# Kernel tuning notes

Measured on AMD Instinct MI355X. Metric: run time of the kernel, lower is better.

Reference implementation:

```python
import jax, jax.numpy as jnp
import numpy as np

N = 100_000   # nodes
E = 1_600_000 # edges (avg degree 16)
IN_DIM = 128
OUT_DIM = 64
NEG_SLOPE = 0.2  # PyG GATConv default


def setup_inputs() -> dict:
    key = jax.random.key(0)
    k_x, k_ei, k_w, k_as, k_ad = jax.random.split(key, 5)
    x = jax.random.normal(k_x, (N, IN_DIM), dtype=jnp.float32)
    edge_index = jax.random.randint(k_ei, (2, E), 0, N, dtype=jnp.int32)
    # GATConv params (heads=1): linear weight, attention vectors, output bias
    W = jax.random.normal(k_w, (IN_DIM, OUT_DIM), dtype=jnp.float32) / np.sqrt(IN_DIM)
    a_src = jax.random.normal(k_as, (OUT_DIM,), dtype=jnp.float32) * 0.1
    a_dst = jax.random.normal(k_ad, (OUT_DIM,), dtype=jnp.float32) * 0.1
    bias = jnp.zeros((OUT_DIM,), dtype=jnp.float32)
    return {"x": x, "edge_index": edge_index, "W": W, "a_src": a_src, "a_dst": a_dst, "bias": bias}


def reference(x, edge_index, W, a_src, a_dst, bias):
    # PyG GATConv, heads=1, add_self_loops=True
    h = x @ W                                   # [N, OUT]
    loop = jnp.arange(N, dtype=edge_index.dtype)
    ei = jnp.concatenate([edge_index, jnp.stack([loop, loop])], axis=1)  # [2, E+N]
    src, dst = ei[0], ei[1]
    # per-node attention logits, gathered per edge
    alpha_s = h @ a_src                         # [N]
    alpha_d = h @ a_dst                         # [N]
    e = alpha_s[src] + alpha_d[dst]             # [E+N]
    e = jnp.where(e > 0, e, NEG_SLOPE * e)      # leaky_relu
    # segment softmax over edges sharing the same destination node
    m = jax.ops.segment_max(e, dst, num_segments=N)   # every node has a self loop
    ex = jnp.exp(e - m[dst])
    s = jax.ops.segment_sum(ex, dst, num_segments=N)
    alpha = ex / s[dst]                         # [E+N]
    # weighted scatter-add of source messages
    out = jax.ops.segment_sum(alpha[:, None] * h[src], dst, num_segments=N)  # [N, OUT]
    return out + bias
```

## Files before the change

### kernel.cpp

```cpp
#include <hip/hip_runtime.h>
#include <hip/hip_bf16.h>

#ifndef NEG_SLOPE
#define NEG_SLOPE 0.2f
#endif

#define GRP_SHIFT 9
#define GRP_SIZE 512
#define NGMAX 256
#define MS_CHUNK 4096
#define BKT_CAP 10240

typedef short bf16x8 __attribute__((ext_vector_type(8)));
typedef float f32x4 __attribute__((ext_vector_type(4)));

__device__ __forceinline__ unsigned short f2bf(float f) {
    union { float f; unsigned int u; } c; c.f = f;
    unsigned int r = (c.u + 0x7FFFu + ((c.u >> 16) & 1u)) >> 16;
    return (unsigned short)r;
}
__device__ __forceinline__ float bf2f(unsigned short u) {
    union { unsigned int u; float f; } c; c.u = ((unsigned int)u) << 16;
    return c.f;
}
__device__ __forceinline__ float bflo(unsigned int u) {
    union { unsigned int u; float f; } c; c.u = u << 16;
    return c.f;
}
__device__ __forceinline__ float bfhi(unsigned int u) {
    union { unsigned int u; float f; } c; c.u = u & 0xffff0000u;
    return c.f;
}

struct GemmSmem {
    unsigned short xb[64 * 136];
    unsigned short wt[64 * 136];
};
struct MsSmem {
    unsigned int pack[MS_CHUNK];
    unsigned char gtag[MS_CHUNK];
    int hist[NGMAX];
    int gb[NGMAX];
    int wsum[4];
};
union FusedSmem {
    GemmSmem g;
    MsSmem m;
};

__global__ __launch_bounds__(256) void gemm_ms_kernel(
    const float* __restrict__ x, const float* __restrict__ W,
    const float* __restrict__ a_src, const float* __restrict__ a_dst,
    unsigned short* __restrict__ hb, float* __restrict__ as_,
    float* __restrict__ ad_, const int* __restrict__ ei,
    int* __restrict__ cursor, unsigned int* __restrict__ pairs,
    int N, int E, int NG, int nchunk)
{
    __shared__ FusedSmem sm;
    const int tid = threadIdx.x;

    if ((int)blockIdx.x < nchunk) {
        unsigned int* ls_pack = sm.m.pack;
        unsigned char* ls_g = sm.m.gtag;
        int* ls_hist = sm.m.hist;
        int* ls_gb = sm.m.gb;
        int* ls_wsum = sm.m.wsum;

        const int cs = (int)blockIdx.x * MS_CHUNK;
        const int n = min(MS_CHUNK, E - cs);
        const int* srcp = ei + cs;
        const int* dstp = ei + E + cs;

        ls_hist[tid] = 0;
        __syncthreads();
        for (int i = tid; i < n; i += 256)
            atomicAdd(&ls_hist[dstp[i] >> GRP_SHIFT], 1);
        __syncthreads();

        const int h = ls_hist[tid];
        const int lane = tid & 63;
        int incl = h;
#pragma unroll
        for (int off = 1; off < 64; off <<= 1) {
            const int t = __shfl_up(incl, off);
            if (lane >= off) incl += t;
        }
        const int wv = tid >> 6;
        if (lane == 63) ls_wsum[wv] = incl;
        __syncthreads();
        int wpre = 0;
        for (int w = 0; w < wv; ++w) wpre += ls_wsum[w];
        const int excl = wpre + incl - h;
        if (tid < NG && h > 0) {
            const int old = atomicAdd(&cursor[tid], h);
            ls_gb[tid] = tid * BKT_CAP + old - excl;
        }
        __syncthreads();
        ls_hist[tid] = excl;
        __syncthreads();

        for (int i = tid; i < n; i += 256) {
            const int src = srcp[i];
            const int dst = dstp[i];
            const int g = dst >> GRP_SHIFT;
            const int idx = atomicAdd(&ls_hist[g], 1);
            ls_pack[idx] = ((unsigned int)src << GRP_SHIFT) | (unsigned int)(dst & (GRP_SIZE - 1));
            ls_g[idx] = (unsigned char)g;
        }
        __syncthreads();

        for (int i = tid; i < n; i += 256) {
            const int g = ls_g[i];
            const int pos = ls_gb[g] + i;
            if (pos < (g + 1) * BKT_CAP)
                pairs[pos] = ls_pack[i];
        }
    } else {
        unsigned short* xb = sm.g.xb;
        unsigned short* wt = sm.g.wt;
        const int r0 = ((int)blockIdx.x - nchunk) * 64;

        for (int idx = tid; idx < 2048; idx += 256) {
            const int r = idx >> 5;
            const int c4 = idx & 31;
            const int row = r0 + r;
            float4 v = make_float4(0.f, 0.f, 0.f, 0.f);
            if (row < N) v = ((const float4*)(x + (size_t)row * 128))[c4];
            ushort4 o;
            o.x = f2bf(v.x); o.y = f2bf(v.y); o.z = f2bf(v.z); o.w = f2bf(v.w);
            *(ushort4*)(xb + r * 136 + c4 * 4) = o;
        }
        {
            const int n = tid & 63;
            const int kb = (tid >> 6) * 32;
            for (int kk = 0; kk < 32; ++kk) {
                const int k = kb + kk;
                wt[n * 136 + k] = f2bf(W[k * 64 + n]);
            }
        }
        __syncthreads();

        const int wv = tid >> 6;
        const int lane = tid & 63;
        const int m16 = lane & 15;
        const int quad = lane >> 4;

        f32x4 acc[4];
#pragma unroll
        for (int ct = 0; ct < 4; ++ct) acc[ct] = (f32x4){0.f, 0.f, 0.f, 0.f};

        const unsigned short* xrow = xb + (wv * 16 + m16) * 136;
#pragma unroll
        for (int kq = 0; kq < 4; ++kq) {
            const int k0 = kq * 32;
            const bf16x8 a = *(const bf16x8*)(xrow + k0 + quad * 8);
#pragma unroll
            for (int ct = 0; ct < 4; ++ct) {
                const bf16x8 b = *(const bf16x8*)(wt + (ct * 16 + m16) * 136 + k0 + quad * 8);
                acc[ct] = __builtin_amdgcn_mfma_f32_16x16x32_bf16(a, b, acc[ct], 0, 0, 0);
            }
        }

#pragma unroll
        for (int ct = 0; ct < 4; ++ct) {
#pragma unroll
            for (int rg = 0; rg < 4; ++rg) {
                const int row = r0 + wv * 16 + quad * 4 + rg;
                if (row < N) hb[(size_t)row * 64 + ct * 16 + m16] = f2bf(acc[ct][rg]);
            }
        }

        float asv[4], adv[4];
#pragma unroll
        for (int ct = 0; ct < 4; ++ct) {
            asv[ct] = a_src[ct * 16 + m16];
            adv[ct] = a_dst[ct * 16 + m16];
        }
#pragma unroll
        for (int rg = 0; rg < 4; ++rg) {
            float ps = acc[0][rg] * asv[0] + acc[1][rg] * asv[1] +
                       acc[2][rg] * asv[2] + acc[3][rg] * asv[3];
            float pd = acc[0][rg] * adv[0] + acc[1][rg] * adv[1] +
                       acc[2][rg] * adv[2] + acc[3][rg] * adv[3];
#pragma unroll
            for (int off = 1; off < 16; off <<= 1) {
                ps += __shfl_xor(ps, off);
                pd += __shfl_xor(pd, off);
            }
            const int row = r0 + wv * 16 + quad * 4 + rg;
            if (m16 == 0 && row < N) { as_[row] = ps; ad_[row] = pd; }
        }
    }
}

__global__ __launch_bounds__(1024) void group_sort_kernel(
    const unsigned int* __restrict__ pairs, const int* __restrict__ cursor,
    unsigned int* __restrict__ meta, int* __restrict__ csr, int N)
{
    __shared__ int sdeg[GRP_SIZE];
    __shared__ int scur[GRP_SIZE];
    __shared__ int swsum[8];
    __shared__ int ssrc[BKT_CAP];
    const int g = blockIdx.x;
    const int tid = threadIdx.x;
    const int eb0 = g * BKT_CAP;
    const int cnt = min(cursor[g], BKT_CAP);

    if (tid < GRP_SIZE) sdeg[tid] = 0;
    __syncthreads();
    for (int i = tid; i < cnt; i += 1024)
        atomicAdd(&sdeg[pairs[eb0 + i] & (GRP_SIZE - 1)], 1);
    __syncthreads();

    int s = 0, incl = 0;
    if (tid < GRP_SIZE) {
        s = sdeg[tid];
        const int lane = tid & 63;
        incl = s;
#pragma unroll
        for (int off = 1; off < 64; off <<= 1) {
            const int t = __shfl_up(incl, off);
            if (lane >= off) incl += t;
        }
        if (lane == 63) swsum[tid >> 6] = incl;
    }
    __syncthreads();
    if (tid < GRP_SIZE) {
        int wpre = 0;
        const int wv = tid >> 6;
        for (int w = 0; w < wv; ++w) wpre += swsum[w];
        const int excl = wpre + incl - s;
        scur[tid] = excl;
        const int node = (g << GRP_SHIFT) + tid;
        if (node < N)
            meta[node] = ((unsigned int)(eb0 + excl) << 10) | (unsigned int)min(s, 1023);
    }
    __syncthreads();

    for (int i = tid; i < cnt; i += 1024) {
        const unsigned int p = pairs[eb0 + i];
        const int idx = atomicAdd(&scur[p & (GRP_SIZE - 1)], 1);
        ssrc[idx] = (int)(p >> GRP_SHIFT);
    }
    __syncthreads();
    for (int i = tid; i < cnt; i += 1024)
        csr[eb0 + i] = ssrc[i];
}

__device__ void aggregate_slow(
    const unsigned short* __restrict__ h, const float* __restrict__ as_,
    const float* __restrict__ ad_, const int* __restrict__ csr,
    const float* __restrict__ bias, float* __restrict__ out,
    int wid, int p0, int deg, int lane)
{
    const float adi = ad_[wid];
    float e0 = as_[wid] + adi;
    e0 = e0 > 0.f ? e0 : NEG_SLOPE * e0;
    float m = e0, ll = 1.f;
    float acc = bf2f(h[(size_t)wid * 64 + lane]);
    const int p1 = p0 + deg;
    for (int p = p0; p < p1; ++p) {
        const int sj = csr[p];
        float ee = as_[sj] + adi;
        ee = ee > 0.f ? ee : NEG_SLOPE * ee;
        const float nm = fmaxf(m, ee);
        const float sc = __expf(m - nm);
        const float pp = __expf(ee - nm);
        ll = ll * sc + pp;
        acc = acc * sc + pp * bf2f(h[(size_t)sj * 64 + lane]);
        m = nm;
    }
    out[(size_t)wid * 64 + lane] = acc / ll + bias[lane];
}

__global__ __launch_bounds__(256) void aggregate_kernel(
    const unsigned short* __restrict__ h, const float* __restrict__ as_,
    const float* __restrict__ ad_, const unsigned int* __restrict__ meta,
    const int* __restrict__ csr, const float* __restrict__ bias,
    float* __restrict__ out, int N)
{
    const int wbase = (blockIdx.x * 256 + threadIdx.x) >> 6;
    const int lane = threadIdx.x & 63;
    const int widA = wbase * 2;
    if (widA >= N) return;
    const int widB = widA + 1;
    const bool hasB = (widB < N);

    const unsigned int mtA = meta[widA];
    const unsigned int mtB = hasB ? meta[widB] : 0u;
    const int p0A = (int)(mtA >> 10), degA = (int)(mtA & 1023u);
    const int p0B = (int)(mtB >> 10), degB = (int)(mtB & 1023u);

    if (degA <= 63 && degB <= 63) {
        const float adiA = ad_[widA];
        const float adiB = hasB ? ad_[widB] : 0.f;
        float e0A = as_[widA] + adiA;
        e0A = e0A > 0.f ? e0A : NEG_SLOPE * e0A;
        float e0B = hasB ? as_[widB] + adiB : 0.f;
        e0B = e0B > 0.f ? e0B : NEG_SLOPE * e0B;

        int sA = widA, sB = hasB ? widB : widA;
        float eA = -1e30f, eB = -1e30f;
        if (lane < degA) {
            sA = csr[p0A + lane];
            const float t = as_[sA] + adiA;
            eA = t > 0.f ? t : NEG_SLOPE * t;
        } else if (lane == degA) {
            eA = e0A;
        }
        if (hasB) {
            if (lane < degB) {
                sB = csr[p0B + lane];
                const float t = as_[sB] + adiB;
                eB = t > 0.f ? t : NEG_SLOPE * t;
            } else if (lane == degB) {
                eB = e0B;
            }
        }

        float mA = eA, mB = eB;
#pragma unroll
        for (int off = 1; off < 64; off <<= 1) {
            mA = fmaxf(mA, __shfl_xor(mA, off));
            mB = fmaxf(mB, __shfl_xor(mB, off));
        }
        const float peA = __expf(eA - mA);
        const float peB = hasB ? __expf(eB - mB) : 0.f;
        float lA = peA, lB = peB;
#pragma unroll
        for (int off = 1; off < 64; off <<= 1) {
            lA += __shfl_xor(lA, off);
            lB += __shfl_xor(lB, off);
        }

        const int half = lane >> 5;
        const int l5 = lane & 31;
        const unsigned int* hb32 = (const unsigned int*)h;
        float a0 = 0.f, a1 = 0.f, b0 = 0.f, b1 = 0.f;
        const int npA = (degA + 2) >> 1;
        const int npB = hasB ? (degB + 2) >> 1 : 0;
        const int npMax = max(npA, npB);

        for (int jp = 0; jp < npMax; jp += 4) {
            const int sl0 = (jp    ) * 2 + half;
            const int sl1 = (jp + 1) * 2 + half;
            const int sl2 = (jp + 2) * 2 + half;
            const int sl3 = (jp + 3) * 2 + half;
            const int sa0 = __shfl(sA, sl0), sa1 = __shfl(sA, sl1);
            const int sa2 = __shfl(sA, sl2), sa3 = __shfl(sA, sl3);
            const int sb0 = __shfl(sB, sl0), sb1 = __shfl(sB, sl1);
            const int sb2 = __shfl(sB, sl2), sb3 = __shfl(sB, sl3);
            const float wa0 = __shfl(peA, sl0), wa1 = __shfl(peA, sl1);
            const float wa2 = __shfl(peA, sl2), wa3 = __shfl(peA, sl3);
            const float wb0 = __shfl(peB, sl0), wb1 = __shfl(peB, sl1);
            const float wb2 = __shfl(peB, sl2), wb3 = __shfl(peB, sl3);
            const unsigned int ua0 = hb32[sa0 * 32 + l5];
            const unsigned int ua1 = hb32[sa1 * 32 + l5];
            const unsigned int ua2 = hb32[sa2 * 32 + l5];
            const unsigned int ua3 = hb32[sa3 * 32 + l5];
            const unsigned int ub0 = hb32[sb0 * 32 + l5];
            const unsigned int ub1 = hb32[sb1 * 32 + l5];
            const unsigned int ub2 = hb32[sb2 * 32 + l5];
            const unsigned int ub3 = hb32[sb3 * 32 + l5];
            a0 += wa0 * bflo(ua0); a1 += wa0 * bfhi(ua0);
            a0 += wa1 * bflo(ua1); a1 += wa1 * bfhi(ua1);
            a0 += wa2 * bflo(ua2); a1 += wa2 * bfhi(ua2);
            a0 += wa3 * bflo(ua3); a1 += wa3 * bfhi(ua3);
            b0 += wb0 * bflo(ub0); b1 += wb0 * bfhi(ub0);
            b0 += wb1 * bflo(ub1); b1 += wb1 * bfhi(ub1);
            b0 += wb2 * bflo(ub2); b1 += wb2 * bfhi(ub2);
            b0 += wb3 * bflo(ub3); b1 += wb3 * bfhi(ub3);
        }
        a0 += __shfl_xor(a0, 32);
        a1 += __shfl_xor(a1, 32);
        b0 += __shfl_xor(b0, 32);
        b1 += __shfl_xor(b1, 32);
        if (half == 0) {
            const float2 bv = ((const float2*)bias)[l5];
            float2 oA;
            oA.x = a0 / lA + bv.x;
            oA.y = a1 / lA + bv.y;
            ((float2*)(out + (size_t)widA * 64))[l5] = oA;
            if (hasB) {
                float2 oB;
                oB.x = b0 / lB + bv.x;
                oB.y = b1 / lB + bv.y;
                ((float2*)(out + (size_t)widB * 64))[l5] = oB;
            }
        }
    } else {
        aggregate_slow(h, as_, ad_, csr, bias, out, widA, p0A, degA, lane);
        if (hasB) aggregate_slow(h, as_, ad_, csr, bias, out, widB, p0B, degB, lane);
    }
}

extern "C" void kernel_launch(void* const* d_in, const int* in_sizes, int n_in,
                              void* d_out, int out_size, void* d_ws, size_t ws_size,
                              hipStream_t stream)
{
    const float* x     = (const float*)d_in[0];
    const int*   ei    = (const int*)d_in[1];
    const float* W     = (const float*)d_in[2];
    const float* a_src = (const float*)d_in[3];
    const float* a_dst = (const float*)d_in[4];
    const float* bias  = (const float*)d_in[5];
    float* out = (float*)d_out;

    const int N = in_sizes[0] / 128;
    const int E = in_sizes[1] / 2;
    const int NG = (N + GRP_SIZE - 1) >> GRP_SHIFT;
    const int nchunk = (E + MS_CHUNK - 1) / MS_CHUNK;
    const int gemmBlocks = (N + 63) / 64;

    unsigned short* hb = (unsigned short*)d_ws;
    float* alpha_s = (float*)(hb + (size_t)N * 64);
    float* alpha_d = alpha_s + N;
    int* cursor = (int*)(alpha_d + N);
    unsigned int* meta = (unsigned int*)(cursor + NG);
    int* csr = (int*)(meta + N);
    unsigned int* pairs = (unsigned int*)(csr + (size_t)NG * BKT_CAP);

    hipMemsetAsync(cursor, 0, (size_t)NG * sizeof(int), stream);
    gemm_ms_kernel<<<nchunk + gemmBlocks, 256, 0, stream>>>(
        x, W, a_src, a_dst, hb, alpha_s, alpha_d, ei, cursor, pairs,
        N, E, NG, nchunk);
    group_sort_kernel<<<NG, 1024, 0, stream>>>(pairs, cursor, meta, csr, N);
    aggregate_kernel<<<(N + 7) / 8, 256, 0, stream>>>(hb, alpha_s, alpha_d, meta,
                                                      csr, bias, out, N);
}
```

Baseline: 180.2 us.

## Fuse group sort into aggregation with per-sub-block shared-memory CSR

Removes the separate group_sort kernel and the global meta/csr arrays. Each aggregation block handles 64 destination nodes, scans its group's whole bucket of pairs, filters the edges that belong to it into shared memory, and counting-sorts them locally before running the same aggregation code. This drops one kernel launch and the global CSR write/read round trip. In exchange, every bucket is read eight times, and occupancy drops to 256 threads per block for the gather phase. SUB_CAP=1600 also caps the edges per 64-node sub-block, and any edges beyond that are silently dropped.

```diff
diff --git a/kernel.cpp b/kernel.cpp
--- a/kernel.cpp
+++ b/kernel.cpp
@@ -10,6 +10,7 @@
 #define NGMAX 256
 #define MS_CHUNK 4096
 #define BKT_CAP 10240
+#define SUB_CAP 1600
 
 typedef short bf16x8 __attribute__((ext_vector_type(8)));
 typedef float f32x4 __attribute__((ext_vector_type(4)));
@@ -193,63 +194,9 @@
     }
 }
 
-__global__ __launch_bounds__(1024) void group_sort_kernel(
-    const unsigned int* __restrict__ pairs, const int* __restrict__ cursor,
-    unsigned int* __restrict__ meta, int* __restrict__ csr, int N)
-{
-    __shared__ int sdeg[GRP_SIZE];
-    __shared__ int scur[GRP_SIZE];
-    __shared__ int swsum[8];
-    __shared__ int ssrc[BKT_CAP];
-    const int g = blockIdx.x;
-    const int tid = threadIdx.x;
-    const int eb0 = g * BKT_CAP;
-    const int cnt = min(cursor[g], BKT_CAP);
-
-    if (tid < GRP_SIZE) sdeg[tid] = 0;
-    __syncthreads();
-    for (int i = tid; i < cnt; i += 1024)
-        atomicAdd(&sdeg[pairs[eb0 + i] & (GRP_SIZE - 1)], 1);
-    __syncthreads();
-
-    int s = 0, incl = 0;
-    if (tid < GRP_SIZE) {
-        s = sdeg[tid];
-        const int lane = tid & 63;
-        incl = s;
-#pragma unroll
-        for (int off = 1; off < 64; off <<= 1) {
-            const int t = __shfl_up(incl, off);
-            if (lane >= off) incl += t;
-        }
-        if (lane == 63) swsum[tid >> 6] = incl;
-    }
-    __syncthreads();
-    if (tid < GRP_SIZE) {
-        int wpre = 0;
-        const int wv = tid >> 6;
-        for (int w = 0; w < wv; ++w) wpre += swsum[w];
-        const int excl = wpre + incl - s;
-        scur[tid] = excl;
-        const int node = (g << GRP_SHIFT) + tid;
-        if (node < N)
-            meta[node] = ((unsigned int)(eb0 + excl) << 10) | (unsigned int)min(s, 1023);
-    }
-    __syncthreads();
-
-    for (int i = tid; i < cnt; i += 1024) {
-        const unsigned int p = pairs[eb0 + i];
-        const int idx = atomicAdd(&scur[p & (GRP_SIZE - 1)], 1);
-        ssrc[idx] = (int)(p >> GRP_SHIFT);
-    }
-    __syncthreads();
-    for (int i = tid; i < cnt; i += 1024)
-        csr[eb0 + i] = ssrc[i];
-}
-
 __device__ void aggregate_slow(
     const unsigned short* __restrict__ h, const float* __restrict__ as_,
-    const float* __restrict__ ad_, const int* __restrict__ csr,
+    const float* __restrict__ ad_, const int* csr,
     const float* __restrict__ bias, float* __restrict__ out,
     int wid, int p0, int deg, int lane)
 {
@@ -273,124 +220,180 @@
     out[(size_t)wid * 64 + lane] = acc / ll + bias[lane];
 }
 
-__global__ __launch_bounds__(256) void aggregate_kernel(
+__global__ __launch_bounds__(256) void sort_agg_kernel(
+    const unsigned int* __restrict__ pairs, const int* __restrict__ cursor,
     const unsigned short* __restrict__ h, const float* __restrict__ as_,
-    const float* __restrict__ ad_, const unsigned int* __restrict__ meta,
-    const int* __restrict__ csr, const float* __restrict__ bias,
+    const float* __restrict__ ad_, const float* __restrict__ bias,
     float* __restrict__ out, int N)
 {
-    const int wbase = (blockIdx.x * 256 + threadIdx.x) >> 6;
-    const int lane = threadIdx.x & 63;
-    const int widA = wbase * 2;
-    if (widA >= N) return;
-    const int widB = widA + 1;
-    const bool hasB = (widB < N);
-
-    const unsigned int mtA = meta[widA];
-    const unsigned int mtB = hasB ? meta[widB] : 0u;
-    const int p0A = (int)(mtA >> 10), degA = (int)(mtA & 1023u);
-    const int p0B = (int)(mtB >> 10), degB = (int)(mtB & 1023u);
-
-    if (degA <= 63 && degB <= 63) {
-        const float adiA = ad_[widA];
-        const float adiB = hasB ? ad_[widB] : 0.f;
-        float e0A = as_[widA] + adiA;
-        e0A = e0A > 0.f ? e0A : NEG_SLOPE * e0A;
-        float e0B = hasB ? as_[widB] + adiB : 0.f;
-        e0B = e0B > 0.f ? e0B : NEG_SLOPE * e0B;
-
-        int sA = widA, sB = hasB ? widB : widA;
-        float eA = -1e30f, eB = -1e30f;
-        if (lane < degA) {
-            sA = csr[p0A + lane];
-            const float t = as_[sA] + adiA;
-            eA = t > 0.f ? t : NEG_SLOPE * t;
-        } else if (lane == degA) {
-            eA = e0A;
-        }
-        if (hasB) {
-            if (lane < degB) {
-                sB = csr[p0B + lane];
-                const float t = as_[sB] + adiB;
-                eB = t > 0.f ? t : NEG_SLOPE * t;
-            } else if (lane == degB) {
-                eB = e0B;
-            }
-        }
-
-        float mA = eA, mB = eB;
+    __shared__ int stmp[SUB_CAP];
+    __shared__ int ssrc[SUB_CAP];
+    __shared__ int sdeg[64];
+    __shared__ int sstart[64];
+    __shared__ int scur[64];
+    __shared__ int stot;
+
+    const int g = (int)blockIdx.x >> 3;
+    const int sub = (int)blockIdx.x & 7;
+    const int base = (g << GRP_SHIFT) + (sub << 6);
+    if (base >= N) return;
+
+    const int tid = threadIdx.x;
+    const int eb0 = g * BKT_CAP;
+    const int cnt = min(cursor[g], BKT_CAP);
+
+    if (tid < 64) sdeg[tid] = 0;
+    if (tid == 0) stot = 0;
+    __syncthreads();
+
+    for (int i = tid; i < cnt; i += 256) {
+        const unsigned int p = pairs[eb0 + i];
+        const int dlow = (int)(p & (GRP_SIZE - 1));
+        if ((dlow >> 6) == sub) {
+            const int idx = atomicAdd(&stot, 1);
+            if (idx < SUB_CAP) {
+                stmp[idx] = (int)((p >> GRP_SHIFT) << 6) | (dlow & 63);
+                atomicAdd(&sdeg[dlow & 63], 1);
+            }
+        }
+    }
+    __syncthreads();
+
+    if (tid < 64) {
+        const int s = sdeg[tid];
+        int incl = s;
 #pragma unroll
         for (int off = 1; off < 64; off <<= 1) {
-            mA = fmaxf(mA, __shfl_xor(mA, off));
-            mB = fmaxf(mB, __shfl_xor(mB, off));
-        }
-        const float peA = __expf(eA - mA);
-        const float peB = hasB ? __expf(eB - mB) : 0.f;
-        float lA = peA, lB = peB;
-#pragma unroll
-        for (int off = 1; off < 64; off <<= 1) {
-            lA += __shfl_xor(lA, off);
-            lB += __shfl_xor(lB, off);
-        }
-
-        const int half = lane >> 5;
-        const int l5 = lane & 31;
-        const unsigned int* hb32 = (const unsigned int*)h;
-        float a0 = 0.f, a1 = 0.f, b0 = 0.f, b1 = 0.f;
-        const int npA = (degA + 2) >> 1;
-        const int npB = hasB ? (degB + 2) >> 1 : 0;
-        const int npMax = max(npA, npB);
-
-        for (int jp = 0; jp < npMax; jp += 4) {
-            const int sl0 = (jp    ) * 2 + half;
-            const int sl1 = (jp + 1) * 2 + half;
-            const int sl2 = (jp + 2) * 2 + half;
-            const int sl3 = (jp + 3) * 2 + half;
-            const int sa0 = __shfl(sA, sl0), sa1 = __shfl(sA, sl1);
-            const int sa2 = __shfl(sA, sl2), sa3 = __shfl(sA, sl3);
-            const int sb0 = __shfl(sB, sl0), sb1 = __shfl(sB, sl1);
-            const int sb2 = __shfl(sB, sl2), sb3 = __shfl(sB, sl3);
-            const float wa0 = __shfl(peA, sl0), wa1 = __shfl(peA, sl1);
-            const float wa2 = __shfl(peA, sl2), wa3 = __shfl(peA, sl3);
-            const float wb0 = __shfl(peB, sl0), wb1 = __shfl(peB, sl1);
-            const float wb2 = __shfl(peB, sl2), wb3 = __shfl(peB, sl3);
-            const unsigned int ua0 = hb32[sa0 * 32 + l5];
-            const unsigned int ua1 = hb32[sa1 * 32 + l5];
-            const unsigned int ua2 = hb32[sa2 * 32 + l5];
-            const unsigned int ua3 = hb32[sa3 * 32 + l5];
-            const unsigned int ub0 = hb32[sb0 * 32 + l5];
-            const unsigned int ub1 = hb32[sb1 * 32 + l5];
-            const unsigned int ub2 = hb32[sb2 * 32 + l5];
-            const unsigned int ub3 = hb32[sb3 * 32 + l5];
-            a0 += wa0 * bflo(ua0); a1 += wa0 * bfhi(ua0);
-            a0 += wa1 * bflo(ua1); a1 += wa1 * bfhi(ua1);
-            a0 += wa2 * bflo(ua2); a1 += wa2 * bfhi(ua2);
-            a0 += wa3 * bflo(ua3); a1 += wa3 * bfhi(ua3);
-            b0 += wb0 * bflo(ub0); b1 += wb0 * bfhi(ub0);
-            b0 += wb1 * bflo(ub1); b1 += wb1 * bfhi(ub1);
-            b0 += wb2 * bflo(ub2); b1 += wb2 * bfhi(ub2);
-            b0 += wb3 * bflo(ub3); b1 += wb3 * bfhi(ub3);
-        }
-        a0 += __shfl_xor(a0, 32);
-        a1 += __shfl_xor(a1, 32);
-        b0 += __shfl_xor(b0, 32);
-        b1 += __shfl_xor(b1, 32);
-        if (half == 0) {
-            const float2 bv = ((const float2*)bias)[l5];
-            float2 oA;
-            oA.x = a0 / lA + bv.x;
-            oA.y = a1 / lA + bv.y;
-            ((float2*)(out + (size_t)widA * 64))[l5] = oA;
+            const int t = __shfl_up(incl, off);
+            if (tid >= off) incl += t;
+        }
+        sstart[tid] = incl - s;
+        scur[tid] = incl - s;
+    }
+    __syncthreads();
+
+    const int tot = min(stot, SUB_CAP);
+    for (int i = tid; i < tot; i += 256) {
+        const int v = stmp[i];
+        const int idx = atomicAdd(&scur[v & 63], 1);
+        ssrc[idx] = v >> 6;
+    }
+    __syncthreads();
+
+    const int wv = tid >> 6;
+    const int lane = tid & 63;
+    const unsigned int* hb32 = (const unsigned int*)h;
+
+    for (int pass = 0; pass < 8; ++pass) {
+        const int nlA = wv * 16 + pass * 2;
+        const int widA = base + nlA;
+        if (widA >= N) continue;
+        const int widB = widA + 1;
+        const bool hasB = (widB < N);
+        const int p0A = sstart[nlA], degA = sdeg[nlA];
+        const int p0B = hasB ? sstart[nlA + 1] : 0;
+        const int degB = hasB ? sdeg[nlA + 1] : 0;
+
+        if (degA <= 63 && degB <= 63) {
+            const float adiA = ad_[widA];
+            const float adiB = hasB ? ad_[widB] : 0.f;
+            float e0A = as_[widA] + adiA;
+            e0A = e0A > 0.f ? e0A : NEG_SLOPE * e0A;
+            float e0B = hasB ? as_[widB] + adiB : 0.f;
+            e0B = e0B > 0.f ? e0B : NEG_SLOPE * e0B;
+
+            int sA = widA, sB = hasB ? widB : widA;
+            float eA = -1e30f, eB = -1e30f;
+            if (lane < degA) {
+                sA = ssrc[p0A + lane];
+                const float t = as_[sA] + adiA;
+                eA = t > 0.f ? t : NEG_SLOPE * t;
+            } else if (lane == degA) {
+                eA = e0A;
+            }
             if (hasB) {
-                float2 oB;
-                oB.x = b0 / lB + bv.x;
-                oB.y = b1 / lB + bv.y;
-                ((float2*)(out + (size_t)widB * 64))[l5] = oB;
-            }
-        }
-    } else {
-        aggregate_slow(h, as_, ad_, csr, bias, out, widA, p0A, degA, lane);
-        if (hasB) aggregate_slow(h, as_, ad_, csr, bias, out, widB, p0B, degB, lane);
+                if (lane < degB) {
+                    sB = ssrc[p0B + lane];
+                    const float t = as_[sB] + adiB;
+                    eB = t > 0.f ? t : NEG_SLOPE * t;
+                } else if (lane == degB) {
+                    eB = e0B;
+                }
+            }
+
+            float mA = eA, mB = eB;
+#pragma unroll
+            for (int off = 1; off < 64; off <<= 1) {
+                mA = fmaxf(mA, __shfl_xor(mA, off));
+                mB = fmaxf(mB, __shfl_xor(mB, off));
+            }
+            const float peA = __expf(eA - mA);
+            const float peB = hasB ? __expf(eB - mB) : 0.f;
+            float lA = peA, lB = peB;
+#pragma unroll
+            for (int off = 1; off < 64; off <<= 1) {
+                lA += __shfl_xor(lA, off);
+                lB += __shfl_xor(lB, off);
+            }
+
+            const int half = lane >> 5;
+            const int l5 = lane & 31;
+            float a0 = 0.f, a1 = 0.f, b0 = 0.f, b1 = 0.f;
+            const int npA = (degA + 2) >> 1;
+            const int npB = hasB ? (degB + 2) >> 1 : 0;
+            const int npMax = max(npA, npB);
+
+            for (int jp = 0; jp < npMax; jp += 4) {
+                const int sl0 = (jp    ) * 2 + half;
+                const int sl1 = (jp + 1) * 2 + half;
+                const int sl2 = (jp + 2) * 2 + half;
+                const int sl3 = (jp + 3) * 2 + half;
+                const int sa0 = __shfl(sA, sl0), sa1 = __shfl(sA, sl1);
+                const int sa2 = __shfl(sA, sl2), sa3 = __shfl(sA, sl3);
+                const int sb0 = __shfl(sB, sl0), sb1 = __shfl(sB, sl1);
+                const int sb2 = __shfl(sB, sl2), sb3 = __shfl(sB, sl3);
+                const float wa0 = __shfl(peA, sl0), wa1 = __shfl(peA, sl1);
+                const float wa2 = __shfl(peA, sl2), wa3 = __shfl(peA, sl3);
+                const float wb0 = __shfl(peB, sl0), wb1 = __shfl(peB, sl1);
+                const float wb2 = __shfl(peB, sl2), wb3 = __shfl(peB, sl3);
+                const unsigned int ua0 = hb32[sa0 * 32 + l5];
+                const unsigned int ua1 = hb32[sa1 * 32 + l5];
+                const unsigned int ua2 = hb32[sa2 * 32 + l5];
+                const unsigned int ua3 = hb32[sa3 * 32 + l5];
+                const unsigned int ub0 = hb32[sb0 * 32 + l5];
+                const unsigned int ub1 = hb32[sb1 * 32 + l5];
+                const unsigned int ub2 = hb32[sb2 * 32 + l5];
+                const unsigned int ub3 = hb32[sb3 * 32 + l5];
+                a0 += wa0 * bflo(ua0); a1 += wa0 * bfhi(ua0);
+                a0 += wa1 * bflo(ua1); a1 += wa1 * bfhi(ua1);
+                a0 += wa2 * bflo(ua2); a1 += wa2 * bfhi(ua2);
+                a0 += wa3 * bflo(ua3); a1 += wa3 * bfhi(ua3);
+                b0 += wb0 * bflo(ub0); b1 += wb0 * bfhi(ub0);
+                b0 += wb1 * bflo(ub1); b1 += wb1 * bfhi(ub1);
+                b0 += wb2 * bflo(ub2); b1 += wb2 * bfhi(ub2);
+                b0 += wb3 * bflo(ub3); b1 += wb3 * bfhi(ub3);
+            }
+            a0 += __shfl_xor(a0, 32);
+            a1 += __shfl_xor(a1, 32);
+            b0 += __shfl_xor(b0, 32);
+            b1 += __shfl_xor(b1, 32);
+            if (half == 0) {
+                const float2 bv = ((const float2*)bias)[l5];
+                float2 oA;
+                oA.x = a0 / lA + bv.x;
+                oA.y = a1 / lA + bv.y;
+                ((float2*)(out + (size_t)widA * 64))[l5] = oA;
+                if (hasB) {
+                    float2 oB;
+                    oB.x = b0 / lB + bv.x;
+                    oB.y = b1 / lB + bv.y;
+                    ((float2*)(out + (size_t)widB * 64))[l5] = oB;
+                }
+            }
+        } else {
+            aggregate_slow(h, as_, ad_, ssrc, bias, out, widA, p0A, degA, lane);
+            if (hasB) aggregate_slow(h, as_, ad_, ssrc, bias, out, widB, p0B, degB, lane);
+        }
     }
 }
 
@@ -416,15 +419,12 @@
     float* alpha_s = (float*)(hb + (size_t)N * 64);
     float* alpha_d = alpha_s + N;
     int* cursor = (int*)(alpha_d + N);
-    unsigned int* meta = (unsigned int*)(cursor + NG);
-    int* csr = (int*)(meta + N);
-    unsigned int* pairs = (unsigned int*)(csr + (size_t)NG * BKT_CAP);
+    unsigned int* pairs = (unsigned int*)(cursor + NG);
 
     hipMemsetAsync(cursor, 0, (size_t)NG * sizeof(int), stream);
     gemm_ms_kernel<<<nchunk + gemmBlocks, 256, 0, stream>>>(
         x, W, a_src, a_dst, hb, alpha_s, alpha_d, ei, cursor, pairs,
         N, E, NG, nchunk);
-    group_sort_kernel<<<NG, 1024, 0, stream>>>(pairs, cursor, meta, csr, N);
-    aggregate_kernel<<<(N + 7) / 8, 256, 0, stream>>>(hb, alpha_s, alpha_d, meta,
-                                                      csr, bias, out, N);
-}
+    sort_agg_kernel<<<NG * 8, 256, 0, stream>>>(pairs, cursor, hb, alpha_s,
+                                                alpha_d, bias, out, N);
+}
```

After: 212.8 us. +18.1%, slower.

## Aggregate one node per wavefront using LDS-staged source indices and weights

Applied to the files above, without the earlier changes.

The aggregate kernel goes from two destination nodes per wavefront, each lane holding a 2-element bf16 pair across two half-waves, to one node per wavefront with one feature per lane. Source indices and unnormalized weights are written to shared memory and read back as int4 broadcasts instead of many per-edge shuffles. The grid doubles to match. This cuts shuffle traffic and the waste of padding to the larger of two degrees, but gathers become 2-byte per lane instead of 4-byte, and there is less memory-level parallelism per wavefront. The LDS slots are written and read by the same wavefront with no barrier, relying on wavefront lockstep.

```diff
diff --git a/kernel.cpp b/kernel.cpp
--- a/kernel.cpp
+++ b/kernel.cpp
@@ -21,14 +21,6 @@
 }
 __device__ __forceinline__ float bf2f(unsigned short u) {
     union { unsigned int u; float f; } c; c.u = ((unsigned int)u) << 16;
-    return c.f;
-}
-__device__ __forceinline__ float bflo(unsigned int u) {
-    union { unsigned int u; float f; } c; c.u = u << 16;
-    return c.f;
-}
-__device__ __forceinline__ float bfhi(unsigned int u) {
-    union { unsigned int u; float f; } c; c.u = u & 0xffff0000u;
     return c.f;
 }
 
@@ -279,118 +271,59 @@
     const int* __restrict__ csr, const float* __restrict__ bias,
     float* __restrict__ out, int N)
 {
-    const int wbase = (blockIdx.x * 256 + threadIdx.x) >> 6;
+    __shared__ int2 slots[4][64];
+    const int wv = threadIdx.x >> 6;
     const int lane = threadIdx.x & 63;
-    const int widA = wbase * 2;
-    if (widA >= N) return;
-    const int widB = widA + 1;
-    const bool hasB = (widB < N);
-
-    const unsigned int mtA = meta[widA];
-    const unsigned int mtB = hasB ? meta[widB] : 0u;
-    const int p0A = (int)(mtA >> 10), degA = (int)(mtA & 1023u);
-    const int p0B = (int)(mtB >> 10), degB = (int)(mtB & 1023u);
-
-    if (degA <= 63 && degB <= 63) {
-        const float adiA = ad_[widA];
-        const float adiB = hasB ? ad_[widB] : 0.f;
-        float e0A = as_[widA] + adiA;
-        e0A = e0A > 0.f ? e0A : NEG_SLOPE * e0A;
-        float e0B = hasB ? as_[widB] + adiB : 0.f;
-        e0B = e0B > 0.f ? e0B : NEG_SLOPE * e0B;
-
-        int sA = widA, sB = hasB ? widB : widA;
-        float eA = -1e30f, eB = -1e30f;
-        if (lane < degA) {
-            sA = csr[p0A + lane];
-            const float t = as_[sA] + adiA;
-            eA = t > 0.f ? t : NEG_SLOPE * t;
-        } else if (lane == degA) {
-            eA = e0A;
-        }
-        if (hasB) {
-            if (lane < degB) {
-                sB = csr[p0B + lane];
-                const float t = as_[sB] + adiB;
-                eB = t > 0.f ? t : NEG_SLOPE * t;
-            } else if (lane == degB) {
-                eB = e0B;
-            }
-        }
-
-        float mA = eA, mB = eB;
-#pragma unroll
-        for (int off = 1; off < 64; off <<= 1) {
-            mA = fmaxf(mA, __shfl_xor(mA, off));
-            mB = fmaxf(mB, __shfl_xor(mB, off));
-        }
-        const float peA = __expf(eA - mA);
-        const float peB = hasB ? __expf(eB - mB) : 0.f;
-        float lA = peA, lB = peB;
-#pragma unroll
-        for (int off = 1; off < 64; off <<= 1) {
-            lA += __shfl_xor(lA, off);
-            lB += __shfl_xor(lB, off);
-        }
-
-        const int half = lane >> 5;
-        const int l5 = lane & 31;
-        const unsigned int* hb32 = (const unsigned int*)h;
-        float a0 = 0.f, a1 = 0.f, b0 = 0.f, b1 = 0.f;
-        const int npA = (degA + 2) >> 1;
-        const int npB = hasB ? (degB + 2) >> 1 : 0;
-        const int npMax = max(npA, npB);
-
-        for (int jp = 0; jp < npMax; jp += 4) {
-            const int sl0 = (jp    ) * 2 + half;
-            const int sl1 = (jp + 1) * 2 + half;
-            const int sl2 = (jp + 2) * 2 + half;
-            const int sl3 = (jp + 3) * 2 + half;
-            const int sa0 = __shfl(sA, sl0), sa1 = __shfl(sA, sl1);
-            const int sa2 = __shfl(sA, sl2), sa3 = __shfl(sA, sl3);
-            const int sb0 = __shfl(sB, sl0), sb1 = __shfl(sB, sl1);
-            const int sb2 = __shfl(sB, sl2), sb3 = __shfl(sB, sl3);
-            const float wa0 = __shfl(peA, sl0), wa1 = __shfl(peA, sl1);
-            const float wa2 = __shfl(peA, sl2), wa3 = __shfl(peA, sl3);
-            const float wb0 = __shfl(peB, sl0), wb1 = __shfl(peB, sl1);
-            const float wb2 = __shfl(peB, sl2), wb3 = __shfl(peB, sl3);
-            const unsigned int ua0 = hb32[sa0 * 32 + l5];
-            const unsigned int ua1 = hb32[sa1 * 32 + l5];
-            const unsigned int ua2 = hb32[sa2 * 32 + l5];
-            const unsigned int ua3 = hb32[sa3 * 32 + l5];
-            const unsigned int ub0 = hb32[sb0 * 32 + l5];
-            const unsigned int ub1 = hb32[sb1 * 32 + l5];
-            const unsigned int ub2 = hb32[sb2 * 32 + l5];
-            const unsigned int ub3 = hb32[sb3 * 32 + l5];
-            a0 += wa0 * bflo(ua0); a1 += wa0 * bfhi(ua0);
-            a0 += wa1 * bflo(ua1); a1 += wa1 * bfhi(ua1);
-            a0 += wa2 * bflo(ua2); a1 += wa2 * bfhi(ua2);
-            a0 += wa3 * bflo(ua3); a1 += wa3 * bfhi(ua3);
-            b0 += wb0 * bflo(ub0); b1 += wb0 * bfhi(ub0);
-            b0 += wb1 * bflo(ub1); b1 += wb1 * bfhi(ub1);
-            b0 += wb2 * bflo(ub2); b1 += wb2 * bfhi(ub2);
-            b0 += wb3 * bflo(ub3); b1 += wb3 * bfhi(ub3);
-        }
-        a0 += __shfl_xor(a0, 32);
-        a1 += __shfl_xor(a1, 32);
-        b0 += __shfl_xor(b0, 32);
-        b1 += __shfl_xor(b1, 32);
-        if (half == 0) {
-            const float2 bv = ((const float2*)bias)[l5];
-            float2 oA;
-            oA.x = a0 / lA + bv.x;
-            oA.y = a1 / lA + bv.y;
-            ((float2*)(out + (size_t)widA * 64))[l5] = oA;
-            if (hasB) {
-                float2 oB;
-                oB.x = b0 / lB + bv.x;
-                oB.y = b1 / lB + bv.y;
-                ((float2*)(out + (size_t)widB * 64))[l5] = oB;
-            }
-        }
+    const int wid = (int)blockIdx.x * 4 + wv;
+    if (wid >= N) return;
+
+    const unsigned int mt = meta[wid];
+    const int p0 = (int)(mt >> 10), deg = (int)(mt & 1023u);
+
+    if (deg <= 63) {
+        const float adi = ad_[wid];
+        float e0 = as_[wid] + adi;
+        e0 = e0 > 0.f ? e0 : NEG_SLOPE * e0;
+
+        int s = wid;
+        float e = -1e30f;
+        if (lane < deg) {
+            s = csr[p0 + lane];
+            const float t = as_[s] + adi;
+            e = t > 0.f ? t : NEG_SLOPE * t;
+        } else if (lane == deg) {
+            e = e0;
+        }
+
+        float m = e;
+#pragma unroll
+        for (int off = 1; off < 64; off <<= 1)
+            m = fmaxf(m, __shfl_xor(m, off));
+        const float pe = __expf(e - m);
+        float l = pe;
+#pragma unroll
+        for (int off = 1; off < 64; off <<= 1)
+            l += __shfl_xor(l, off);
+
+        slots[wv][lane] = make_int2(s, __float_as_int(pe));
+
+        float acc = 0.f;
+        const int ecnt4 = (deg + 4) & ~3;
+        for (int j = 0; j < ecnt4; j += 4) {
+            const int4 qa = *(const int4*)&slots[wv][j];
+            const int4 qb = *(const int4*)&slots[wv][j + 2];
+            const unsigned short u0 = h[(size_t)qa.x * 64 + lane];
+            const unsigned short u1 = h[(size_t)qa.z * 64 + lane];
+            const unsigned short u2 = h[(size_t)qb.x * 64 + lane];
+            const unsigned short u3 = h[(size_t)qb.z * 64 + lane];
+            acc += __int_as_float(qa.y) * bf2f(u0);
+            acc += __int_as_float(qa.w) * bf2f(u1);
+            acc += __int_as_float(qb.y) * bf2f(u2);
+            acc += __int_as_float(qb.w) * bf2f(u3);
+        }
+        out[(size_t)wid * 64 + lane] = acc / l + bias[lane];
     } else {
-        aggregate_slow(h, as_, ad_, csr, bias, out, widA, p0A, degA, lane);
-        if (hasB) aggregate_slow(h, as_, ad_, csr, bias, out, widB, p0B, degB, lane);
+        aggregate_slow(h, as_, ad_, csr, bias, out, wid, p0, deg, lane);
     }
 }
 
@@ -425,6 +358,6 @@
         x, W, a_src, a_dst, hb, alpha_s, alpha_d, ei, cursor, pairs,
         N, E, NG, nchunk);
     group_sort_kernel<<<NG, 1024, 0, stream>>>(pairs, cursor, meta, csr, N);
-    aggregate_kernel<<<(N + 7) / 8, 256, 0, stream>>>(hb, alpha_s, alpha_d, meta,
+    aggregate_kernel<<<(N + 3) / 4, 256, 0, stream>>>(hb, alpha_s, alpha_d, meta,
                                                       csr, bias, out, N);
 }
```

After: 184.6 us. 2.4% more time.

## Split fused GEMM/multisplit kernel and pre-convert W to bf16 once

Applied to the files above, without the earlier changes.

Splits the fused edge-bucketing and GEMM kernel into two separate kernels. The bucketing kernel gains one extra block that converts and transposes W to bf16 a single time into a workspace buffer. The GEMM then reads W fragments straight from global memory (cached) instead of each block rebuilding a transposed copy in LDS. This removes the redundant per-block W conversion and the shared union that inflated LDS per block, at the cost of an extra launch and no longer overlapping the GEMM with the bucketing work.

```diff
diff --git a/kernel.cpp b/kernel.cpp
--- a/kernel.cpp
+++ b/kernel.cpp
@@ -32,10 +32,6 @@
     return c.f;
 }
 
-struct GemmSmem {
-    unsigned short xb[64 * 136];
-    unsigned short wt[64 * 136];
-};
 struct MsSmem {
     unsigned int pack[MS_CHUNK];
     unsigned char gtag[MS_CHUNK];
@@ -43,153 +39,78 @@
     int gb[NGMAX];
     int wsum[4];
 };
-union FusedSmem {
-    GemmSmem g;
-    MsSmem m;
-};
-
-__global__ __launch_bounds__(256) void gemm_ms_kernel(
-    const float* __restrict__ x, const float* __restrict__ W,
-    const float* __restrict__ a_src, const float* __restrict__ a_dst,
-    unsigned short* __restrict__ hb, float* __restrict__ as_,
-    float* __restrict__ ad_, const int* __restrict__ ei,
-    int* __restrict__ cursor, unsigned int* __restrict__ pairs,
-    int N, int E, int NG, int nchunk)
-{
-    __shared__ FusedSmem sm;
+
+__global__ __launch_bounds__(256) void ms_kernel(
+    const int* __restrict__ ei, const float* __restrict__ W,
+    unsigned short* __restrict__ wb, int* __restrict__ cursor,
+    unsigned int* __restrict__ pairs, int E, int NG, int nchunk)
+{
+    __shared__ MsSmem sm;
     const int tid = threadIdx.x;
 
-    if ((int)blockIdx.x < nchunk) {
-        unsigned int* ls_pack = sm.m.pack;
-        unsigned char* ls_g = sm.m.gtag;
-        int* ls_hist = sm.m.hist;
-        int* ls_gb = sm.m.gb;
-        int* ls_wsum = sm.m.wsum;
-
-        const int cs = (int)blockIdx.x * MS_CHUNK;
-        const int n = min(MS_CHUNK, E - cs);
-        const int* srcp = ei + cs;
-        const int* dstp = ei + E + cs;
-
-        ls_hist[tid] = 0;
-        __syncthreads();
-        for (int i = tid; i < n; i += 256)
-            atomicAdd(&ls_hist[dstp[i] >> GRP_SHIFT], 1);
-        __syncthreads();
-
-        const int h = ls_hist[tid];
-        const int lane = tid & 63;
-        int incl = h;
-#pragma unroll
-        for (int off = 1; off < 64; off <<= 1) {
-            const int t = __shfl_up(incl, off);
-            if (lane >= off) incl += t;
-        }
-        const int wv = tid >> 6;
-        if (lane == 63) ls_wsum[wv] = incl;
-        __syncthreads();
-        int wpre = 0;
-        for (int w = 0; w < wv; ++w) wpre += ls_wsum[w];
-        const int excl = wpre + incl - h;
-        if (tid < NG && h > 0) {
-            const int old = atomicAdd(&cursor[tid], h);
-            ls_gb[tid] = tid * BKT_CAP + old - excl;
-        }
-        __syncthreads();
-        ls_hist[tid] = excl;
-        __syncthreads();
-
-        for (int i = tid; i < n; i += 256) {
-            const int src = srcp[i];
-            const int dst = dstp[i];
-            const int g = dst >> GRP_SHIFT;
-            const int idx = atomicAdd(&ls_hist[g], 1);
-            ls_pack[idx] = ((unsigned int)src << GRP_SHIFT) | (unsigned int)(dst & (GRP_SIZE - 1));
-            ls_g[idx] = (unsigned char)g;
-        }
-        __syncthreads();
-
-        for (int i = tid; i < n; i += 256) {
-            const int g = ls_g[i];
-            const int pos = ls_gb[g] + i;
-            if (pos < (g + 1) * BKT_CAP)
-                pairs[pos] = ls_pack[i];
-        }
-    } else {
-        unsigned short* xb = sm.g.xb;
-        unsigned short* wt = sm.g.wt;
-        const int r0 = ((int)blockIdx.x - nchunk) * 64;
-
-        for (int idx = tid; idx < 2048; idx += 256) {
-            const int r = idx >> 5;
-            const int c4 = idx & 31;
-            const int row = r0 + r;
-            float4 v = make_float4(0.f, 0.f, 0.f, 0.f);
-            if (row < N) v = ((const float4*)(x + (size_t)row * 128))[c4];
-            ushort4 o;
-            o.x = f2bf(v.x); o.y = f2bf(v.y); o.z = f2bf(v.z); o.w = f2bf(v.w);
-            *(ushort4*)(xb + r * 136 + c4 * 4) = o;
-        }
-        {
-            const int n = tid & 63;
-            const int kb = (tid >> 6) * 32;
-            for (int kk = 0; kk < 32; ++kk) {
-                const int k = kb + kk;
-                wt[n * 136 + k] = f2bf(W[k * 64 + n]);
-            }
-        }
-        __syncthreads();
-
-        const int wv = tid >> 6;
-        const int lane = tid & 63;
-        const int m16 = lane & 15;
-        const int quad = lane >> 4;
-
-        f32x4 acc[4];
-#pragma unroll
-        for (int ct = 0; ct < 4; ++ct) acc[ct] = (f32x4){0.f, 0.f, 0.f, 0.f};
-
-        const unsigned short* xrow = xb + (wv * 16 + m16) * 136;
-#pragma unroll
-        for (int kq = 0; kq < 4; ++kq) {
-            const int k0 = kq * 32;
-            const bf16x8 a = *(const bf16x8*)(xrow + k0 + quad * 8);
-#pragma unroll
-            for (int ct = 0; ct < 4; ++ct) {
-                const bf16x8 b = *(const bf16x8*)(wt + (ct * 16 + m16) * 136 + k0 + quad * 8);
-                acc[ct] = __builtin_amdgcn_mfma_f32_16x16x32_bf16(a, b, acc[ct], 0, 0, 0);
-            }
-        }
-
-#pragma unroll
-        for (int ct = 0; ct < 4; ++ct) {
-#pragma unroll
-            for (int rg = 0; rg < 4; ++rg) {
-                const int row = r0 + wv * 16 + quad * 4 + rg;
-                if (row < N) hb[(size_t)row * 64 + ct * 16 + m16] = f2bf(acc[ct][rg]);
-            }
-        }
-
-        float asv[4], adv[4];
-#pragma unroll
-        for (int ct = 0; ct < 4; ++ct) {
-            asv[ct] = a_src[ct * 16 + m16];
-            adv[ct] = a_dst[ct * 16 + m16];
-        }
-#pragma unroll
-        for (int rg = 0; rg < 4; ++rg) {
-            float ps = acc[0][rg] * asv[0] + acc[1][rg] * asv[1] +
-                       acc[2][rg] * asv[2] + acc[3][rg] * asv[3];
-            float pd = acc[0][rg] * adv[0] + acc[1][rg] * adv[1] +
-                       acc[2][rg] * adv[2] + acc[3][rg] * adv[3];
-#pragma unroll
-            for (int off = 1; off < 16; off <<= 1) {
-                ps += __shfl_xor(ps, off);
-                pd += __shfl_xor(pd, off);
-            }
-            const int row = r0 + wv * 16 + quad * 4 + rg;
-            if (m16 == 0 && row < N) { as_[row] = ps; ad_[row] = pd; }
-        }
+    if ((int)blockIdx.x == nchunk) {
+        for (int idx = tid; idx < 8192; idx += 256) {
+            const int n = idx >> 7;
+            const int k = idx & 127;
+            wb[idx] = f2bf(W[k * 64 + n]);
+        }
+        return;
+    }
+
+    unsigned int* ls_pack = sm.pack;
+    unsigned char* ls_g = sm.gtag;
+    int* ls_hist = sm.hist;
+    int* ls_gb = sm.gb;
+    int* ls_wsum = sm.wsum;
+
+    const int cs = (int)blockIdx.x * MS_CHUNK;
+    const int n = min(MS_CHUNK, E - cs);
+    const int* srcp = ei + cs;
+    const int* dstp = ei + E + cs;
+
+    ls_hist[tid] = 0;
+    __syncthreads();
+    for (int i = tid; i < n; i += 256)
+        atomicAdd(&ls_hist[dstp[i] >> GRP_SHIFT], 1);
+    __syncthreads();
+
+    const int h = ls_hist[tid];
+    const int lane = tid & 63;
+    int incl = h;
+#pragma unroll
+    for (int off = 1; off < 64; off <<= 1) {
+        const int t = __shfl_up(incl, off);
+        if (lane >= off) incl += t;
+    }
+    const int wv = tid >> 6;
+    if (lane == 63) ls_wsum[wv] = incl;
+    __syncthreads();
+    int wpre = 0;
+    for (int w = 0; w < wv; ++w) wpre += ls_wsum[w];
+    const int excl = wpre + incl - h;
+    if (tid < NG && h > 0) {
+        const int old = atomicAdd(&cursor[tid], h);
+        ls_gb[tid] = tid * BKT_CAP + old - excl;
+    }
+    __syncthreads();
+    ls_hist[tid] = excl;
+    __syncthreads();
+
+    for (int i = tid; i < n; i += 256) {
+        const int src = srcp[i];
+        const int dst = dstp[i];
+        const int g = dst >> GRP_SHIFT;
+        const int idx = atomicAdd(&ls_hist[g], 1);
+        ls_pack[idx] = ((unsigned int)src << GRP_SHIFT) | (unsigned int)(dst & (GRP_SIZE - 1));
+        ls_g[idx] = (unsigned char)g;
+    }
+    __syncthreads();
+
+    for (int i = tid; i < n; i += 256) {
+        const int g = ls_g[i];
+        const int pos = ls_gb[g] + i;
+        if (pos < (g + 1) * BKT_CAP)
+            pairs[pos] = ls_pack[i];
     }
 }
 
@@ -245,6 +166,80 @@
     __syncthreads();
     for (int i = tid; i < cnt; i += 1024)
         csr[eb0 + i] = ssrc[i];
+}
+
+__global__ __launch_bounds__(256) void gemm_kernel(
+    const float* __restrict__ x, const unsigned short* __restrict__ wb,
+    const float* __restrict__ a_src, const float* __restrict__ a_dst,
+    unsigned short* __restrict__ hb, float* __restrict__ as_,
+    float* __restrict__ ad_, int N)
+{
+    __shared__ unsigned short xb[64 * 136];
+    const int tid = threadIdx.x;
+    const int r0 = (int)blockIdx.x * 64;
+
+    for (int idx = tid; idx < 2048; idx += 256) {
+        const int r = idx >> 5;
+        const int c4 = idx & 31;
+        const int row = r0 + r;
+        float4 v = make_float4(0.f, 0.f, 0.f, 0.f);
+        if (row < N) v = ((const float4*)(x + (size_t)row * 128))[c4];
+        ushort4 o;
+        o.x = f2bf(v.x); o.y = f2bf(v.y); o.z = f2bf(v.z); o.w = f2bf(v.w);
+        *(ushort4*)(xb + r * 136 + c4 * 4) = o;
+    }
+    __syncthreads();
+
+    const int wv = tid >> 6;
+    const int lane = tid & 63;
+    const int m16 = lane & 15;
+    const int quad = lane >> 4;
+
+    f32x4 acc[4];
+#pragma unroll
+    for (int ct = 0; ct < 4; ++ct) acc[ct] = (f32x4){0.f, 0.f, 0.f, 0.f};
+
+    const unsigned short* xrow = xb + (wv * 16 + m16) * 136;
+#pragma unroll
+    for (int kq = 0; kq < 4; ++kq) {
+        const int k0 = kq * 32;
+        const bf16x8 a = *(const bf16x8*)(xrow + k0 + quad * 8);
+#pragma unroll
+        for (int ct = 0; ct < 4; ++ct) {
+            const bf16x8 b = *(const bf16x8*)(wb + (ct * 16 + m16) * 128 + k0 + quad * 8);
+            acc[ct] = __builtin_amdgcn_mfma_f32_16x16x32_bf16(a, b, acc[ct], 0, 0, 0);
+        }
+    }
+
+#pragma unroll
+    for (int ct = 0; ct < 4; ++ct) {
+#pragma unroll
+        for (int rg = 0; rg < 4; ++rg) {
+            const int row = r0 + wv * 16 + quad * 4 + rg;
+            if (row < N) hb[(size_t)row * 64 + ct * 16 + m16] = f2bf(acc[ct][rg]);
+        }
+    }
+
+    float asv[4], adv[4];
+#pragma unroll
+    for (int ct = 0; ct < 4; ++ct) {
+        asv[ct] = a_src[ct * 16 + m16];
+        adv[ct] = a_dst[ct * 16 + m16];
+    }
+#pragma unroll
+    for (int rg = 0; rg < 4; ++rg) {
+        float ps = acc[0][rg] * asv[0] + acc[1][rg] * asv[1] +
+                   acc[2][rg] * asv[2] + acc[3][rg] * asv[3];
+        float pd = acc[0][rg] * adv[0] + acc[1][rg] * adv[1] +
+                   acc[2][rg] * adv[2] + acc[3][rg] * adv[3];
+#pragma unroll
+        for (int off = 1; off < 16; off <<= 1) {
+            ps += __shfl_xor(ps, off);
+            pd += __shfl_xor(pd, off);
+        }
+        const int row = r0 + wv * 16 + quad * 4 + rg;
+        if (m16 == 0 && row < N) { as_[row] = ps; ad_[row] = pd; }
+    }
 }
 
 __device__ void aggregate_slow(
@@ -419,12 +414,14 @@
     unsigned int* meta = (unsigned int*)(cursor + NG);
     int* csr = (int*)(meta + N);
     unsigned int* pairs = (unsigned int*)(csr + (size_t)NG * BKT_CAP);
+    unsigned short* wbuf = (unsigned short*)(pairs + (size_t)NG * BKT_CAP);
 
     hipMemsetAsync(cursor, 0, (size_t)NG * sizeof(int), stream);
-    gemm_ms_kernel<<<nchunk + gemmBlocks, 256, 0, stream>>>(
-        x, W, a_src, a_dst, hb, alpha_s, alpha_d, ei, cursor, pairs,
-        N, E, NG, nchunk);
+    ms_kernel<<<nchunk + 1, 256, 0, stream>>>(ei, W, wbuf, cursor, pairs,
+                                              E, NG, nchunk);
     group_sort_kernel<<<NG, 1024, 0, stream>>>(pairs, cursor, meta, csr, N);
+    gemm_kernel<<<gemmBlocks, 256, 0, stream>>>(x, wbuf, a_src, a_dst, hb,
+                                                alpha_s, alpha_d, N);
     aggregate_kernel<<<(N + 7) / 8, 256, 0, stream>>>(hb, alpha_s, alpha_d, meta,
                                                       csr, bias, out, N);
 }
```

Result: slower. 191.9 us (+6.5%).
